# Optimization experiments

Hardware: AMD Instinct MI355X
Metric: run time of the kernel (lower is better)

The kernel has to match this reference:

```python
import jax, jax.numpy as jnp
import numpy as np

D_MODEL = 1024
N_HEADS = 16
D_FF = 4096
LN_EPS = 1e-5


def _layernorm(x, g, b):
    mu = jnp.mean(x, axis=-1, keepdims=True)
    var = jnp.var(x, axis=-1, keepdims=True)
    return (x - mu) * jax.lax.rsqrt(var + LN_EPS) * g + b


def setup_inputs() -> dict:
    key = jax.random.key(0)
    ks = jax.random.split(key, 10)
    N, B, C, F = 2048, 4, D_MODEL, D_FF
    s = lambda fan_in: 1.0 / np.sqrt(fan_in)
    return {
        "src": jax.random.normal(ks[0], (N, B, C), dtype=jnp.float32),
        "ln_g": jnp.ones((C,), jnp.float32),
        "ln_b": jnp.zeros((C,), jnp.float32),
        "w_qkv": jax.random.normal(ks[1], (C, 3 * C), jnp.float32) * s(C),
        "w_proj": jax.random.normal(ks[2], (C, C), jnp.float32) * s(C),
        "b_proj": jnp.zeros((C,), jnp.float32),
        "w1": jax.random.normal(ks[3], (C, F), jnp.float32) * s(C),
        "b1": jnp.zeros((F,), jnp.float32),
        "w2": jax.random.normal(ks[4], (F, C), jnp.float32) * s(F),
        "b2": jnp.zeros((C,), jnp.float32),
    }


def reference(src, ln_g, ln_b, w_qkv, w_proj, b_proj, w1, b1, w2, b2):
    N, B, C = src.shape
    H = N_HEADS
    hd = C // H
    scale = hd ** -0.5

    # pre-norm (norm_first=True)
    x = _layernorm(src, ln_g, ln_b)

    # qkv: (N,B,3C) -> (N,B,3,H,hd) -> permute(2,1,3,0,4) = (3,B,H,N,hd)
    qkv = (x @ w_qkv).reshape(N, B, 3, H, hd).transpose(2, 1, 3, 0, 4)
    q, k, v = qkv[0], qkv[1], qkv[2]  # (B,H,N,hd)

    attn = jax.nn.softmax(jnp.einsum("bhnd,bhmd->bhnm", q, k) * scale, axis=-1)
    o = jnp.einsum("bhnm,bhmd->bhnd", attn, v)  # (B,H,N,hd)
    # faithful to original: transpose(0,2) -> (N,H,B,hd), then reshape (N,B,C)
    o = o.transpose(2, 1, 0, 3).reshape(N, B, C)
    o = o @ w_proj + b_proj

    src = src + o
    # post_norm is Identity (norm_first=True)
    h = jax.nn.gelu(src @ w1 + b1, approximate=False)
    src = src + (h @ w2 + b2)
    return src
```

## Files before the change

kernel.cpp:

```cpp
#include <hip/hip_runtime.h>
#include <hip/hip_bf16.h>
#include <math.h>

typedef unsigned short u16;
typedef __attribute__((ext_vector_type(4))) unsigned short u16x4;
typedef __attribute__((ext_vector_type(8))) short short8;
typedef __attribute__((ext_vector_type(4))) float f32x4;
typedef __attribute__((ext_vector_type(16))) float f32x16;

__device__ __forceinline__ void gl_lds16(const void* g, void* s) {
  __builtin_amdgcn_global_load_lds((const __attribute__((address_space(1))) void*)g,
                                   (__attribute__((address_space(3))) void*)s, 16, 0, 0);
}

__device__ __forceinline__ u16 f2bf(float f) {
  union { float f; unsigned u; } a; a.f = f;
  unsigned r = a.u + 0x7fff + ((a.u >> 16) & 1);
  return (u16)(r >> 16);
}

__device__ __forceinline__ unsigned pk2(float a, float b) {
  union { __hip_bfloat162 h; unsigned u; } cv;
  cv.h = __float22bfloat162_rn(make_float2(a, b));
  return cv.u;
}

__device__ __forceinline__ short8 mk8(unsigned a, unsigned b, unsigned c, unsigned d) {
  union { unsigned u[4]; short8 v; } cv;
  cv.u[0] = a; cv.u[1] = b; cv.u[2] = c; cv.u[3] = d; return cv.v;
}

__device__ __forceinline__ short8 scale8(short8 v, float s) {
  short8 r;
  #pragma unroll
  for (int i = 0; i < 8; ++i) {
    union { float f; unsigned u; } a; a.u = ((unsigned)(u16)v[i]) << 16;
    r[i] = (short)f2bf(a.f * s);
  }
  return r;
}

__device__ __forceinline__ f32x16 z16() {
  f32x16 z;
  #pragma unroll
  for (int i = 0; i < 16; ++i) z[i] = 0.f;
  return z;
}

__global__ __launch_bounds__(256) void ln_kernel(const float* __restrict__ src,
                                                 const float* __restrict__ g,
                                                 const float* __restrict__ b,
                                                 u16* __restrict__ out) {
  int row = blockIdx.x;
  int t = threadIdx.x;
  const float4* s4 = (const float4*)(src + (size_t)row * 1024);
  float4 x = s4[t];
  float s1 = x.x + x.y + x.z + x.w;
  float s2 = x.x * x.x + x.y * x.y + x.z * x.z + x.w * x.w;
  for (int m = 32; m; m >>= 1) { s1 += __shfl_xor(s1, m); s2 += __shfl_xor(s2, m); }
  __shared__ float red[8];
  int w = t >> 6, lane = t & 63;
  if (lane == 0) { red[w] = s1; red[4 + w] = s2; }
  __syncthreads();
  float tot  = red[0] + red[1] + red[2] + red[3];
  float tot2 = red[4] + red[5] + red[6] + red[7];
  float mean = tot * (1.0f / 1024.0f);
  float var  = tot2 * (1.0f / 1024.0f) - mean * mean;
  float rs = rsqrtf(var + 1e-5f);
  float4 gg = ((const float4*)g)[t];
  float4 bb = ((const float4*)b)[t];
  u16x4 o;
  o[0] = f2bf((x.x - mean) * rs * gg.x + bb.x);
  o[1] = f2bf((x.y - mean) * rs * gg.y + bb.y);
  o[2] = f2bf((x.z - mean) * rs * gg.z + bb.z);
  o[3] = f2bf((x.w - mean) * rs * gg.w + bb.w);
  ((u16x4*)(out + (size_t)row * 1024))[t] = o;
}

__global__ __launch_bounds__(256) void tcast_kernel(const float* __restrict__ in,
                                                    u16* __restrict__ out, int K, int N) {
  __shared__ float tt[64][65];
  int t = threadIdx.x;
  int n0 = blockIdx.x * 64, k0 = blockIdx.y * 64;
  #pragma unroll
  for (int s = 0; s < 4; ++s) {
    int idx = s * 256 + t;
    int r = idx >> 4, c4 = idx & 15;
    float4 v = *(const float4*)(in + (size_t)(k0 + r) * N + n0 + c4 * 4);
    tt[r][c4 * 4 + 0] = v.x; tt[r][c4 * 4 + 1] = v.y;
    tt[r][c4 * 4 + 2] = v.z; tt[r][c4 * 4 + 3] = v.w;
  }
  __syncthreads();
  #pragma unroll
  for (int s = 0; s < 4; ++s) {
    int idx = s * 256 + t;
    int nr = idx >> 4, kc = idx & 15;
    u16x4 o;
    o[0] = f2bf(tt[kc * 4 + 0][nr]);
    o[1] = f2bf(tt[kc * 4 + 1][nr]);
    o[2] = f2bf(tt[kc * 4 + 2][nr]);
    o[3] = f2bf(tt[kc * 4 + 3][nr]);
    *(u16x4*)(out + (size_t)(n0 + nr) * K + k0 + kc * 4) = o;
  }
}

__global__ __launch_bounds__(256) void vtrans_kernel(const u16* __restrict__ qkv,
                                                     u16* __restrict__ vt) {
  __shared__ u16 tile[64][66];
  int t = threadIdx.x;
  int nt = blockIdx.x, bh = blockIdx.y;
  int bb = bh >> 4, hh = bh & 15;
  int n0 = nt * 64;
  #pragma unroll
  for (int s = 0; s < 2; ++s) {
    int idx = s * 256 + t;
    int i = idx >> 3, c = idx & 7;
    union { short8 v; unsigned u[4]; } cv;
    cv.v = *(const short8*)(qkv + (size_t)((n0 + i) * 4 + bb) * 3072 + 2048 + hh * 64 + c * 8);
    unsigned* dst = (unsigned*)&tile[i][c * 8];
    dst[0] = cv.u[0]; dst[1] = cv.u[1]; dst[2] = cv.u[2]; dst[3] = cv.u[3];
  }
  __syncthreads();
  #pragma unroll
  for (int s = 0; s < 2; ++s) {
    int idx = s * 256 + t;
    int d = idx >> 3, ch = idx & 7;
    union { u16 e[8]; short8 v; } ov;
    #pragma unroll
    for (int j = 0; j < 8; ++j) {
      int P = ch * 8 + j;
      int q = P & 15, blk = q >> 2;
      int bp = ((blk & 1) << 1) | (blk >> 1);
      int src = (P & ~15) | (bp << 2) | (q & 3);
      ov.e[j] = tile[src][d];
    }
    *(short8*)(vt + ((size_t)(bh * 64 + d)) * 2048 + n0 + ch * 8) = ov.v;
  }
}

template <int EPI>
__global__ __launch_bounds__(256, 2) void gemm_kernel(
    const u16* __restrict__ A, const u16* __restrict__ Bt,
    int M, int N, int K,
    const float* __restrict__ bias, const float* __restrict__ resid,
    float* __restrict__ outf, u16* __restrict__ outh, int ldo) {
  __shared__ u16 lA[128 * 32];
  __shared__ u16 lB[128 * 32];
  int t = threadIdx.x, w = t >> 6, lane = t & 63;
  int bm = blockIdx.x, bn = blockIdx.y;
  int wm = (w >> 1) * 64, wn = (w & 1) * 64;
  int am = lane & 15, ag = lane >> 4;
  f32x4 acc[4][4];
  #pragma unroll
  for (int i = 0; i < 4; ++i)
    #pragma unroll
    for (int j = 0; j < 4; ++j)
      #pragma unroll
      for (int r = 0; r < 4; ++r) acc[i][j][r] = 0.f;

  const size_t rowA0 = (size_t)bm * 128, colB0 = (size_t)bn * 128;

  for (int k0 = 0; k0 < K; k0 += 32) {
    #pragma unroll
    for (int s = 0; s < 2; ++s) {
      int c = s * 256 + w * 64 + lane;
      int row = c >> 2, cc = c & 3;
      int scc = cc ^ ((row >> 1) & 3);
      gl_lds16(A  + (rowA0 + row) * K + k0 + scc * 8, (char*)lA + (size_t)(s * 256 + w * 64) * 16);
      gl_lds16(Bt + (colB0 + row) * K + k0 + scc * 8, (char*)lB + (size_t)(s * 256 + w * 64) * 16);
    }
    __syncthreads();
    short8 af[4], bfr[4];
    #pragma unroll
    for (int i = 0; i < 4; ++i) {
      int row = wm + i * 16 + am;
      int ch = ag ^ ((row >> 1) & 3);
      af[i] = *(const short8*)(lA + row * 32 + ch * 8);
    }
    #pragma unroll
    for (int j = 0; j < 4; ++j) {
      int row = wn + j * 16 + am;
      int ch = ag ^ ((row >> 1) & 3);
      bfr[j] = *(const short8*)(lB + row * 32 + ch * 8);
    }
    #pragma unroll
    for (int i = 0; i < 4; ++i)
      #pragma unroll
      for (int j = 0; j < 4; ++j)
        acc[i][j] = __builtin_amdgcn_mfma_f32_16x16x32_bf16(af[i], bfr[j], acc[i][j], 0, 0, 0);
    __syncthreads();
  }

  #pragma unroll
  for (int i = 0; i < 4; ++i) {
    #pragma unroll
    for (int j = 0; j < 4; ++j) {
      #pragma unroll
      for (int r = 0; r < 4; ++r) {
        int grow = (int)rowA0 + wm + i * 16 + ag * 4 + r;
        int gcol = (int)colB0 + wn + j * 16 + am;
        float v = acc[i][j][r];
        if (EPI == 0) {
          outh[(size_t)grow * ldo + gcol] = f2bf(v);
        } else if (EPI == 1) {
          size_t idx = (size_t)grow * 1024 + gcol;
          float y = resid[idx] + v + bias[gcol];
          outf[idx] = y;
          outh[idx] = f2bf(y);
        } else if (EPI == 2) {
          float x = v + bias[gcol];
          float ge = 0.5f * x * (1.0f + erff(x * 0.70710678118654752f));
          outh[(size_t)grow * ldo + gcol] = f2bf(ge);
        } else {
          size_t idx = (size_t)grow * 1024 + gcol;
          outf[idx] = resid[idx] + v + bias[gcol];
        }
      }
    }
  }
}

#define SOFTMAX(S0, S1, MM, LL, OA, OB, WDS) { \
  float smax = S0[0]; \
  _Pragma("unroll") for (int i = 1; i < 16; ++i) smax = fmaxf(smax, S0[i]); \
  _Pragma("unroll") for (int i = 0; i < 16; ++i) smax = fmaxf(smax, S1[i]); \
  smax = fmaxf(smax, __shfl_xor(smax, 32)); \
  if (!__all(smax <= MM + 11.5416f)) { \
    float mn = fmaxf(MM, smax); float al = exp2f(MM - mn); \
    LL *= al; \
    _Pragma("unroll") for (int i = 0; i < 16; ++i) { OA[i] *= al; OB[i] *= al; } \
    MM = mn; \
  } \
  float rsum = 0.f; \
  _Pragma("unroll") for (int j = 0; j < 8; ++j) { \
    float ea = exp2f(S0[2*j] - MM), eb = exp2f(S0[2*j+1] - MM); \
    rsum += ea + eb; WDS[j] = pk2(ea, eb); } \
  _Pragma("unroll") for (int j = 0; j < 8; ++j) { \
    float ea = exp2f(S1[2*j] - MM), eb = exp2f(S1[2*j+1] - MM); \
    rsum += ea + eb; WDS[8+j] = pk2(ea, eb); } \
  rsum += __shfl_xor(rsum, 32); \
  LL += rsum; }

__global__ __launch_bounds__(256, 3) void attn_kernel(const u16* __restrict__ qkv,
                                                      const u16* __restrict__ Vt,
                                                      u16* __restrict__ Omix) {
  const int t = threadIdx.x, w = t >> 6, lane = t & 63, l31 = lane & 31, hi = lane >> 5;
  const int i = blockIdx.x;
  const int orig = (i & 7) * 64 + (i >> 3);
  const int qb = orig & 7, bh = orig >> 3;
  const int bb = bh >> 4, hh = bh & 15;
  const float SC = 0.125f * 1.44269504f;

  short8 qf[2][4];
  #pragma unroll
  for (int qt = 0; qt < 2; ++qt)
    #pragma unroll
    for (int kc = 0; kc < 4; ++kc) {
      int qn = qb * 256 + w * 64 + qt * 32 + l31;
      const u16* p = qkv + (size_t)(qn * 4 + bb) * 3072 + hh * 64 + kc * 16 + hi * 8;
      qf[qt][kc] = scale8(*(const short8*)p, SC);
    }

  const u16* kbase = qkv + (size_t)bb * 3072 + 1024 + hh * 64;
  const u16* vbase = Vt + (size_t)(bh * 64) * 2048;

  float m0 = -1e30f, l0 = 0.f, m1 = -1e30f, l1 = 0.f;
  f32x16 o00 = z16(), o01 = z16(), o10 = z16(), o11 = z16();
  const f32x16 ZED = z16();

  for (int kt = 0; kt < 32; ++kt) {
    const int n0 = kt * 64;

    short8 kf0[4], kf1[4];
    #pragma unroll
    for (int kc = 0; kc < 4; ++kc) {
      kf0[kc] = *(const short8*)(kbase + (size_t)(n0 + l31) * 4 * 3072 + (2 * kc + hi) * 8);
      kf1[kc] = *(const short8*)(kbase + (size_t)(n0 + 32 + l31) * 4 * 3072 + (2 * kc + hi) * 8);
    }

    f32x16 sA = __builtin_amdgcn_mfma_f32_32x32x16_bf16(kf0[0], qf[0][0], ZED, 0, 0, 0);
    f32x16 sB = __builtin_amdgcn_mfma_f32_32x32x16_bf16(kf1[0], qf[0][0], ZED, 0, 0, 0);
    #pragma unroll
    for (int kc = 1; kc < 4; ++kc) {
      sA = __builtin_amdgcn_mfma_f32_32x32x16_bf16(kf0[kc], qf[0][kc], sA, 0, 0, 0);
      sB = __builtin_amdgcn_mfma_f32_32x32x16_bf16(kf1[kc], qf[0][kc], sB, 0, 0, 0);
    }
    unsigned wd0[16];
    SOFTMAX(sA, sB, m0, l0, o00, o01, wd0);

    f32x16 sC = __builtin_amdgcn_mfma_f32_32x32x16_bf16(kf0[0], qf[1][0], ZED, 0, 0, 0);
    f32x16 sD = __builtin_amdgcn_mfma_f32_32x32x16_bf16(kf1[0], qf[1][0], ZED, 0, 0, 0);
    #pragma unroll
    for (int kc = 1; kc < 4; ++kc) {
      sC = __builtin_amdgcn_mfma_f32_32x32x16_bf16(kf0[kc], qf[1][kc], sC, 0, 0, 0);
      sD = __builtin_amdgcn_mfma_f32_32x32x16_bf16(kf1[kc], qf[1][kc], sD, 0, 0, 0);
    }
    unsigned wd1[16];
    SOFTMAX(sC, sD, m1, l1, o10, o11, wd1);

    short8 vf0[4], vf1[4];
    #pragma unroll
    for (int st = 0; st < 4; ++st) {
      vf0[st] = *(const short8*)(vbase + (size_t)l31 * 2048 + n0 + (2 * st + hi) * 8);
      vf1[st] = *(const short8*)(vbase + (size_t)(32 + l31) * 2048 + n0 + (2 * st + hi) * 8);
    }

    #pragma unroll
    for (int st = 0; st < 4; ++st) {
      short8 bA = mk8(wd0[4 * st], wd0[4 * st + 1], wd0[4 * st + 2], wd0[4 * st + 3]);
      o00 = __builtin_amdgcn_mfma_f32_32x32x16_bf16(vf0[st], bA, o00, 0, 0, 0);
      o01 = __builtin_amdgcn_mfma_f32_32x32x16_bf16(vf1[st], bA, o01, 0, 0, 0);
      short8 bB = mk8(wd1[4 * st], wd1[4 * st + 1], wd1[4 * st + 2], wd1[4 * st + 3]);
      o10 = __builtin_amdgcn_mfma_f32_32x32x16_bf16(vf0[st], bB, o10, 0, 0, 0);
      o11 = __builtin_amdgcn_mfma_f32_32x32x16_bf16(vf1[st], bB, o11, 0, 0, 0);
    }
  }

  float r0 = 1.f / l0, r1 = 1.f / l1;
  #pragma unroll
  for (int qt = 0; qt < 2; ++qt) {
    float rl = qt ? r1 : r0;
    int qn = qb * 256 + w * 64 + qt * 32 + l31;
    size_t base = ((size_t)(qn * 4 + (hh >> 2))) * 1024 + (hh & 3) * 256 + bb * 64;
    #pragma unroll
    for (int dt = 0; dt < 2; ++dt) {
      #pragma unroll
      for (int reg = 0; reg < 16; ++reg) {
        int d = dt * 32 + (reg & 3) + 8 * (reg >> 2) + 4 * hi;
        float val = (qt ? (dt ? o11[reg] : o10[reg]) : (dt ? o01[reg] : o00[reg])) * rl;
        Omix[base + d] = f2bf(val);
      }
    }
  }
}

extern "C" void kernel_launch(void* const* d_in, const int* in_sizes, int n_in,
                              void* d_out, int out_size, void* d_ws, size_t ws_size,
                              hipStream_t stream) {
  const float* src    = (const float*)d_in[0];
  const float* ln_g   = (const float*)d_in[1];
  const float* ln_b   = (const float*)d_in[2];
  const float* w_qkv  = (const float*)d_in[3];
  const float* w_proj = (const float*)d_in[4];
  const float* b_proj = (const float*)d_in[5];
  const float* w1     = (const float*)d_in[6];
  const float* b1     = (const float*)d_in[7];
  const float* w2     = (const float*)d_in[8];
  const float* b2     = (const float*)d_in[9];

  char* ws = (char*)d_ws;
  u16* wqkvT  = (u16*)(ws + 0);
  u16* wprojT = (u16*)(ws + 6291456);
  u16* w1T    = (u16*)(ws + 8388608);
  u16* w2T    = (u16*)(ws + 16777216);
  u16* xln    = (u16*)(ws + 25165824);
  u16* Omix   = xln;
  u16* qkv    = (u16*)(ws + 41943040);
  u16* Vtb    = (u16*)(ws + 92274688);
  u16* hbuf   = (u16*)(ws + 41943040);
  u16* ybf    = (u16*)(ws + 109051904);
  float* yf   = (float*)d_out;

  dim3 blk(256);
  tcast_kernel<<<dim3(48, 16), blk, 0, stream>>>(w_qkv, wqkvT, 1024, 3072);
  tcast_kernel<<<dim3(16, 16), blk, 0, stream>>>(w_proj, wprojT, 1024, 1024);
  tcast_kernel<<<dim3(64, 16), blk, 0, stream>>>(w1, w1T, 1024, 4096);
  tcast_kernel<<<dim3(16, 64), blk, 0, stream>>>(w2, w2T, 4096, 1024);
  ln_kernel<<<8192, blk, 0, stream>>>(src, ln_g, ln_b, xln);

  gemm_kernel<0><<<dim3(64, 24), blk, 0, stream>>>(xln, wqkvT, 8192, 3072, 1024,
      nullptr, nullptr, nullptr, qkv, 3072);

  vtrans_kernel<<<dim3(32, 64), blk, 0, stream>>>(qkv, Vtb);

  attn_kernel<<<512, blk, 0, stream>>>(qkv, Vtb, Omix);

  gemm_kernel<1><<<dim3(64, 8), blk, 0, stream>>>(Omix, wprojT, 8192, 1024, 1024,
      b_proj, src, yf, ybf, 1024);

  gemm_kernel<2><<<dim3(64, 32), blk, 0, stream>>>(ybf, w1T, 8192, 4096, 1024,
      b1, nullptr, nullptr, hbuf, 4096);

  gemm_kernel<3><<<dim3(64, 8), blk, 0, stream>>>(hbuf, w2T, 8192, 1024, 4096,
      b2, yf, (float*)d_out, nullptr, 1024);
}
```

Measured before the change: 635.0 us.

## Halve per-wave query rows in attention kernel and double grid size

Each wave now handles 32 query rows instead of 64, so a block covers 128 queries and the grid grows from 512 to 1024 blocks. V fragment loads are hoisted next to the K loads at the start of each key tile. The intent is to cut accumulator register pressure and raise occupancy and parallelism, hiding global-load latency for K/V. In exchange, each K/V fragment loaded from global memory is reused across half as many query rows, so total K/V load traffic doubles.

Result: slower. 692.1 us (+9.0%).

```diff
diff --git a/kernel.cpp b/kernel.cpp
--- a/kernel.cpp
+++ b/kernel.cpp
@@ -241,95 +241,72 @@
   rsum += __shfl_xor(rsum, 32); \
   LL += rsum; }
 
-__global__ __launch_bounds__(256, 3) void attn_kernel(const u16* __restrict__ qkv,
-                                                      const u16* __restrict__ Vt,
-                                                      u16* __restrict__ Omix) {
+__global__ __launch_bounds__(256) void attn_kernel(const u16* __restrict__ qkv,
+                                                   const u16* __restrict__ Vt,
+                                                   u16* __restrict__ Omix) {
   const int t = threadIdx.x, w = t >> 6, lane = t & 63, l31 = lane & 31, hi = lane >> 5;
   const int i = blockIdx.x;
-  const int orig = (i & 7) * 64 + (i >> 3);
-  const int qb = orig & 7, bh = orig >> 3;
+  const int orig = (i & 7) * 128 + (i >> 3);
+  const int qb = orig & 15, bh = orig >> 4;
   const int bb = bh >> 4, hh = bh & 15;
   const float SC = 0.125f * 1.44269504f;
 
-  short8 qf[2][4];
-  #pragma unroll
-  for (int qt = 0; qt < 2; ++qt)
-    #pragma unroll
-    for (int kc = 0; kc < 4; ++kc) {
-      int qn = qb * 256 + w * 64 + qt * 32 + l31;
-      const u16* p = qkv + (size_t)(qn * 4 + bb) * 3072 + hh * 64 + kc * 16 + hi * 8;
-      qf[qt][kc] = scale8(*(const short8*)p, SC);
-    }
+  const int qn = qb * 128 + w * 32 + l31;
+  short8 qf[4];
+  #pragma unroll
+  for (int kc = 0; kc < 4; ++kc) {
+    const u16* p = qkv + (size_t)(qn * 4 + bb) * 3072 + hh * 64 + kc * 16 + hi * 8;
+    qf[kc] = scale8(*(const short8*)p, SC);
+  }
 
   const u16* kbase = qkv + (size_t)bb * 3072 + 1024 + hh * 64;
   const u16* vbase = Vt + (size_t)(bh * 64) * 2048;
 
-  float m0 = -1e30f, l0 = 0.f, m1 = -1e30f, l1 = 0.f;
-  f32x16 o00 = z16(), o01 = z16(), o10 = z16(), o11 = z16();
-  const f32x16 ZED = z16();
+  float m0 = -1e30f, l0 = 0.f;
+  f32x16 o0 = z16(), o1 = z16();
 
   for (int kt = 0; kt < 32; ++kt) {
     const int n0 = kt * 64;
 
-    short8 kf0[4], kf1[4];
+    short8 kf0[4], kf1[4], vf0[4], vf1[4];
     #pragma unroll
     for (int kc = 0; kc < 4; ++kc) {
-      kf0[kc] = *(const short8*)(kbase + (size_t)(n0 + l31) * 4 * 3072 + (2 * kc + hi) * 8);
-      kf1[kc] = *(const short8*)(kbase + (size_t)(n0 + 32 + l31) * 4 * 3072 + (2 * kc + hi) * 8);
-    }
-
-    f32x16 sA = __builtin_amdgcn_mfma_f32_32x32x16_bf16(kf0[0], qf[0][0], ZED, 0, 0, 0);
-    f32x16 sB = __builtin_amdgcn_mfma_f32_32x32x16_bf16(kf1[0], qf[0][0], ZED, 0, 0, 0);
-    #pragma unroll
-    for (int kc = 1; kc < 4; ++kc) {
-      sA = __builtin_amdgcn_mfma_f32_32x32x16_bf16(kf0[kc], qf[0][kc], sA, 0, 0, 0);
-      sB = __builtin_amdgcn_mfma_f32_32x32x16_bf16(kf1[kc], qf[0][kc], sB, 0, 0, 0);
-    }
-    unsigned wd0[16];
-    SOFTMAX(sA, sB, m0, l0, o00, o01, wd0);
-
-    f32x16 sC = __builtin_amdgcn_mfma_f32_32x32x16_bf16(kf0[0], qf[1][0], ZED, 0, 0, 0);
-    f32x16 sD = __builtin_amdgcn_mfma_f32_32x32x16_bf16(kf1[0], qf[1][0], ZED, 0, 0, 0);
-    #pragma unroll
-    for (int kc = 1; kc < 4; ++kc) {
-      sC = __builtin_amdgcn_mfma_f32_32x32x16_bf16(kf0[kc], qf[1][kc], sC, 0, 0, 0);
-      sD = __builtin_amdgcn_mfma_f32_32x32x16_bf16(kf1[kc], qf[1][kc], sD, 0, 0, 0);
-    }
-    unsigned wd1[16];
-    SOFTMAX(sC, sD, m1, l1, o10, o11, wd1);
-
-    short8 vf0[4], vf1[4];
+      kf0[kc] = *(const short8*)(kbase + (size_t)(n0 + l31) * 12288 + (2 * kc + hi) * 8);
+      kf1[kc] = *(const short8*)(kbase + (size_t)(n0 + 32 + l31) * 12288 + (2 * kc + hi) * 8);
+    }
     #pragma unroll
     for (int st = 0; st < 4; ++st) {
       vf0[st] = *(const short8*)(vbase + (size_t)l31 * 2048 + n0 + (2 * st + hi) * 8);
       vf1[st] = *(const short8*)(vbase + (size_t)(32 + l31) * 2048 + n0 + (2 * st + hi) * 8);
     }
 
+    f32x16 sA = z16(), sB = z16();
+    #pragma unroll
+    for (int kc = 0; kc < 4; ++kc) {
+      sA = __builtin_amdgcn_mfma_f32_32x32x16_bf16(kf0[kc], qf[kc], sA, 0, 0, 0);
+      sB = __builtin_amdgcn_mfma_f32_32x32x16_bf16(kf1[kc], qf[kc], sB, 0, 0, 0);
+    }
+
+    unsigned wd[16];
+    SOFTMAX(sA, sB, m0, l0, o0, o1, wd);
+
     #pragma unroll
     for (int st = 0; st < 4; ++st) {
-      short8 bA = mk8(wd0[4 * st], wd0[4 * st + 1], wd0[4 * st + 2], wd0[4 * st + 3]);
-      o00 = __builtin_amdgcn_mfma_f32_32x32x16_bf16(vf0[st], bA, o00, 0, 0, 0);
-      o01 = __builtin_amdgcn_mfma_f32_32x32x16_bf16(vf1[st], bA, o01, 0, 0, 0);
-      short8 bB = mk8(wd1[4 * st], wd1[4 * st + 1], wd1[4 * st + 2], wd1[4 * st + 3]);
-      o10 = __builtin_amdgcn_mfma_f32_32x32x16_bf16(vf0[st], bB, o10, 0, 0, 0);
-      o11 = __builtin_amdgcn_mfma_f32_32x32x16_bf16(vf1[st], bB, o11, 0, 0, 0);
-    }
-  }
-
-  float r0 = 1.f / l0, r1 = 1.f / l1;
-  #pragma unroll
-  for (int qt = 0; qt < 2; ++qt) {
-    float rl = qt ? r1 : r0;
-    int qn = qb * 256 + w * 64 + qt * 32 + l31;
-    size_t base = ((size_t)(qn * 4 + (hh >> 2))) * 1024 + (hh & 3) * 256 + bb * 64;
-    #pragma unroll
-    for (int dt = 0; dt < 2; ++dt) {
-      #pragma unroll
-      for (int reg = 0; reg < 16; ++reg) {
-        int d = dt * 32 + (reg & 3) + 8 * (reg >> 2) + 4 * hi;
-        float val = (qt ? (dt ? o11[reg] : o10[reg]) : (dt ? o01[reg] : o00[reg])) * rl;
-        Omix[base + d] = f2bf(val);
-      }
+      short8 bA = mk8(wd[4 * st], wd[4 * st + 1], wd[4 * st + 2], wd[4 * st + 3]);
+      o0 = __builtin_amdgcn_mfma_f32_32x32x16_bf16(vf0[st], bA, o0, 0, 0, 0);
+      o1 = __builtin_amdgcn_mfma_f32_32x32x16_bf16(vf1[st], bA, o1, 0, 0, 0);
+    }
+  }
+
+  const float rl = 1.f / l0;
+  const size_t base = ((size_t)(qn * 4 + (hh >> 2))) * 1024 + (hh & 3) * 256 + bb * 64;
+  #pragma unroll
+  for (int dt = 0; dt < 2; ++dt) {
+    #pragma unroll
+    for (int reg = 0; reg < 16; ++reg) {
+      int d = dt * 32 + (reg & 3) + 8 * (reg >> 2) + 4 * hi;
+      float val = (dt ? o1[reg] : o0[reg]) * rl;
+      Omix[base + d] = f2bf(val);
     }
   }
 }
@@ -373,7 +350,7 @@
 
   vtrans_kernel<<<dim3(32, 64), blk, 0, stream>>>(qkv, Vtb);
 
-  attn_kernel<<<512, blk, 0, stream>>>(qkv, Vtb, Omix);
+  attn_kernel<<<1024, blk, 0, stream>>>(qkv, Vtb, Omix);
 
   gemm_kernel<1><<<dim3(64, 8), blk, 0, stream>>>(Omix, wprojT, 8192, 1024, 1024,
       b_proj, src, yf, ybf, 1024);
```
